# Optimization experiments

Measured on AMD Instinct MI355X. Metric: run time of the kernel, lower is better.

Reference implementation:

```python
import jax, jax.numpy as jnp
import numpy as np

N_NODES = 100000
N_EDGES = 600000
FEAT_DIM = 128


def setup_inputs() -> dict:
    key = jax.random.key(0)
    k_x, k_e, k_w1, k_b1, k_w2, k_b2 = jax.random.split(key, 6)
    x = jax.random.normal(k_x, (N_NODES, FEAT_DIM), dtype=jnp.float32)
    edge_index = jax.random.randint(k_e, (2, N_EDGES), 0, N_NODES, dtype=jnp.int64)
    # nn.Linear default init: U(-1/sqrt(fan_in), 1/sqrt(fan_in))
    lim1 = 1.0 / np.sqrt(2 * FEAT_DIM)
    lim2 = 1.0 / np.sqrt(FEAT_DIM)
    W1 = jax.random.uniform(k_w1, (2 * FEAT_DIM, FEAT_DIM), minval=-lim1, maxval=lim1, dtype=jnp.float32)
    b1 = jax.random.uniform(k_b1, (FEAT_DIM,), minval=-lim1, maxval=lim1, dtype=jnp.float32)
    W2 = jax.random.uniform(k_w2, (FEAT_DIM, 1), minval=-lim2, maxval=lim2, dtype=jnp.float32)
    b2 = jax.random.uniform(k_b2, (1,), minval=-lim2, maxval=lim2, dtype=jnp.float32)
    return {"x": x, "edge_index": edge_index, "W1": W1, "b1": b1, "W2": W2, "b2": b2}


def reference(x, edge_index, W1, b1, W2, b2):
    row, col = edge_index[0], edge_index[1]
    # gather endpoint features and concat -> [E, 2*feat_dim]
    edge_feat = jnp.concatenate([x[row], x[col]], axis=1)
    h = jax.nn.relu(edge_feat @ W1 + b1)  # [E, feat_dim]
    return jax.nn.sigmoid(h @ W2 + b2)    # [E, 1]
```

## Files before the change

kernel.cpp:

```cpp
#include <hip/hip_runtime.h>
#include <stdint.h>

#define N_NODES 100000
#define N_EDGES 600000
#define FEAT 128

typedef __attribute__((ext_vector_type(8))) short short8;
typedef __attribute__((ext_vector_type(4))) float floatx4;

__device__ __forceinline__ short f2bf(float f) {
    unsigned u = __builtin_bit_cast(unsigned, f);
    u = (u + 0x7FFFu + ((u >> 16) & 1u)) >> 16;
    return (short)u;
}
__device__ __forceinline__ float bf2f(short s) {
    unsigned u = ((unsigned)(unsigned short)s) << 16;
    return __builtin_bit_cast(float, u);
}

__global__ void cvt_w_kernel(const float* __restrict__ w1, short* __restrict__ wbt) {
    int i = blockIdx.x * 256 + threadIdx.x;
    int n = i >> 7, k = i & 127;
    float f = (n < FEAT) ? w1[k * FEAT + n] : w1[(FEAT + k) * FEAT + (n - FEAT)];
    wbt[i] = f2bf(f);
}

__global__ __launch_bounds__(256, 2) void node_gemm_kernel(
    const float* __restrict__ x, const short* __restrict__ wbt, short* __restrict__ y)
{
    __shared__ short lds_b[16 * 256 * 8];

    const int tid = threadIdx.x;
    for (int j = tid; j < 16 * 256; j += 256) {
        int n = j & 255, c = j >> 8;
        short8 v = *(const short8*)(wbt + n * 128 + c * 8);
        *(short8*)(lds_b + ((c << 8) + n) * 8) = v;
    }
    __syncthreads();

    const int lane = tid & 63;
    const int wave = tid >> 6;
    const int nl = lane & 15;
    const int q  = lane >> 4;
    const int m0 = blockIdx.x * 64 + wave * 16;

    const int node = m0 + nl;
    const int nsrc = (node < N_NODES) ? node : 0;
    short8 a[4];
#pragma unroll
    for (int s = 0; s < 4; ++s) {
        const float* p = x + (size_t)nsrc * FEAT + s * 32 + q * 8;
        short8 av;
#pragma unroll
        for (int j = 0; j < 8; ++j) av[j] = f2bf(p[j]);
        a[s] = av;
    }

    floatx4 acc[16];
#pragma unroll
    for (int nt = 0; nt < 16; ++nt) acc[nt] = (floatx4)(0.0f);

#pragma unroll
    for (int s = 0; s < 4; ++s) {
        const int crow = (s * 4 + q) << 8;
#pragma unroll
        for (int nt = 0; nt < 16; ++nt) {
            short8 bf = *(const short8*)(lds_b + ((crow + nt * 16 + nl) << 3));
            acc[nt] = __builtin_amdgcn_mfma_f32_16x16x32_bf16(a[s], bf, acc[nt], 0, 0, 0);
        }
    }

#pragma unroll
    for (int r = 0; r < 4; ++r) {
        int m = m0 + q * 4 + r;
        if (m >= N_NODES) continue;
        short* yr = y + (size_t)m * 256 + nl;
#pragma unroll
        for (int nt = 0; nt < 16; ++nt) yr[nt * 16] = f2bf(acc[nt][r]);
    }
}

__global__ __launch_bounds__(256) void edge_kernel(
    const short* __restrict__ y, const int* __restrict__ eidx,
    const float* __restrict__ b1, const float* __restrict__ w2,
    const float* __restrict__ b2, float* __restrict__ out)
{
    const int l = threadIdx.x & 15;

    float b1r[8], w2r[8];
#pragma unroll
    for (int j = 0; j < 8; ++j) {
        b1r[j] = b1[l * 8 + j];
        w2r[j] = w2[l * 8 + j];
    }
    const float bias2 = b2[0];

    const int slot   = blockIdx.x * 16 + (threadIdx.x >> 4);
    const int stride = gridDim.x * 16;

    for (int e = slot; e < N_EDGES; e += stride) {
        const int r = eidx[e];
        const int c = eidx[N_EDGES + e];

        short8 uu = *(const short8*)(y + (size_t)r * 256 + l * 8);
        short8 vv = *(const short8*)(y + (size_t)c * 256 + 128 + l * 8);

        float p = 0.0f;
#pragma unroll
        for (int j = 0; j < 8; ++j) {
            float h = bf2f(uu[j]) + bf2f(vv[j]) + b1r[j];
            p = fmaf(fmaxf(h, 0.0f), w2r[j], p);
        }
        p += __shfl_xor(p, 1);
        p += __shfl_xor(p, 2);
        p += __shfl_xor(p, 4);
        p += __shfl_xor(p, 8);

        if (l == 0) out[e] = 1.0f / (1.0f + __expf(-(p + bias2)));
    }
}

extern "C" void kernel_launch(void* const* d_in, const int* in_sizes, int n_in,
                              void* d_out, int out_size, void* d_ws, size_t ws_size,
                              hipStream_t stream) {
    const float* x  = (const float*)d_in[0];
    const int*   ei = (const int*)d_in[1];
    const float* W1 = (const float*)d_in[2];
    const float* b1 = (const float*)d_in[3];
    const float* W2 = (const float*)d_in[4];
    const float* b2 = (const float*)d_in[5];
    float* out = (float*)d_out;

    short* ybf = (short*)d_ws;
    short* wbt = ybf + (size_t)N_NODES * 256;

    cvt_w_kernel<<<32768 / 256, 256, 0, stream>>>(W1, wbt);

    int mblocks = (N_NODES + 63) / 64;
    node_gemm_kernel<<<mblocks, 256, 0, stream>>>(x, wbt, ybf);

    edge_kernel<<<2048, 256, 0, stream>>>(ybf, ei, b1, W2, b2, out);
}
```

Baseline: 166.1 us.

## Persistent split-N node GEMM with prefetch, swizzled LDS, and batched edge gathers

The node GEMM becomes a persistent grid where each block owns one 128-column half of W1. It keeps that half in an XOR-swizzled LDS layout, prefetches the next tile's x rows into registers during the MFMAs, and writes output with vectorized 4-wide stores with b1 folded in. The edge kernel drops the per-edge bias add and software-pipelines gathers four edges at a time, loading the next batch before computing the current one. This trades higher register pressure and a smaller per-block GEMM for better latency hiding and fewer LDS bank conflicts.

```diff
diff --git a/kernel.cpp b/kernel.cpp
--- a/kernel.cpp
+++ b/kernel.cpp
@@ -4,8 +4,12 @@
 #define N_NODES 100000
 #define N_EDGES 600000
 #define FEAT 128
+#define NTILES 1563
+#define NTASKS (NTILES * 2)
+#define GRID_G 1024
 
 typedef __attribute__((ext_vector_type(8))) short short8;
+typedef __attribute__((ext_vector_type(4))) short sv4;
 typedef __attribute__((ext_vector_type(4))) float floatx4;
 
 __device__ __forceinline__ short f2bf(float f) {
@@ -25,98 +29,158 @@
     wbt[i] = f2bf(f);
 }
 
-__global__ __launch_bounds__(256, 2) void node_gemm_kernel(
-    const float* __restrict__ x, const short* __restrict__ wbt, short* __restrict__ y)
+__global__ __launch_bounds__(256, 4) void node_gemm_kernel(
+    const float* __restrict__ x, const short* __restrict__ wbt,
+    const float* __restrict__ b1, short* __restrict__ y)
 {
-    __shared__ short lds_b[16 * 256 * 8];
-
-    const int tid = threadIdx.x;
-    for (int j = tid; j < 16 * 256; j += 256) {
-        int n = j & 255, c = j >> 8;
-        short8 v = *(const short8*)(wbt + n * 128 + c * 8);
-        *(short8*)(lds_b + ((c << 8) + n) * 8) = v;
-    }
-    __syncthreads();
-
+    __shared__ short lds_b[128 * 128];
+
+    const int tid  = threadIdx.x;
     const int lane = tid & 63;
     const int wave = tid >> 6;
-    const int nl = lane & 15;
-    const int q  = lane >> 4;
-    const int m0 = blockIdx.x * 64 + wave * 16;
-
-    const int node = m0 + nl;
-    const int nsrc = (node < N_NODES) ? node : 0;
-    short8 a[4];
-#pragma unroll
-    for (int s = 0; s < 4; ++s) {
-        const float* p = x + (size_t)nsrc * FEAT + s * 32 + q * 8;
-        short8 av;
-#pragma unroll
-        for (int j = 0; j < 8; ++j) av[j] = f2bf(p[j]);
-        a[s] = av;
-    }
-
-    floatx4 acc[16];
-#pragma unroll
-    for (int nt = 0; nt < 16; ++nt) acc[nt] = (floatx4)(0.0f);
-
-#pragma unroll
-    for (int s = 0; s < 4; ++s) {
-        const int crow = (s * 4 + q) << 8;
-#pragma unroll
-        for (int nt = 0; nt < 16; ++nt) {
-            short8 bf = *(const short8*)(lds_b + ((crow + nt * 16 + nl) << 3));
-            acc[nt] = __builtin_amdgcn_mfma_f32_16x16x32_bf16(a[s], bf, acc[nt], 0, 0, 0);
-        }
-    }
-
-#pragma unroll
-    for (int r = 0; r < 4; ++r) {
-        int m = m0 + q * 4 + r;
-        if (m >= N_NODES) continue;
-        short* yr = y + (size_t)m * 256 + nl;
-#pragma unroll
-        for (int nt = 0; nt < 16; ++nt) yr[nt * 16] = f2bf(acc[nt][r]);
+    const int nl   = lane & 15;
+    const int q    = lane >> 4;
+    const int swz  = nl & 7;
+    const int nh   = blockIdx.x & 1;
+
+#pragma unroll
+    for (int j0 = 0; j0 < 2048; j0 += 256) {
+        int j = j0 + tid;
+        int n = j >> 4, kc = j & 15;
+        short8 v = *(const short8*)(wbt + (nh * 128 + n) * 128 + kc * 8);
+        *(short8*)(lds_b + n * 128 + ((kc ^ (n & 7)) << 3)) = v;
+    }
+    __syncthreads();
+
+    int task = blockIdx.x;
+    float xf[32];
+    {
+        int node = (task >> 1) * 64 + wave * 16 + nl;
+        int nsrc = (node < N_NODES) ? node : 0;
+        const float* p = x + (size_t)nsrc * FEAT + q * 8;
+#pragma unroll
+        for (int s = 0; s < 4; ++s)
+#pragma unroll
+            for (int j = 0; j < 8; ++j) xf[s * 8 + j] = p[s * 32 + j];
+    }
+
+    for (; task < NTASKS; task += GRID_G) {
+        const int node = (task >> 1) * 64 + wave * 16 + nl;
+
+        short8 a[4];
+#pragma unroll
+        for (int s = 0; s < 4; ++s) {
+            short8 av;
+#pragma unroll
+            for (int j = 0; j < 8; ++j) av[j] = f2bf(xf[s * 8 + j]);
+            a[s] = av;
+        }
+
+        int task2 = task + GRID_G;
+        if (task2 < NTASKS) {
+            int node2 = (task2 >> 1) * 64 + wave * 16 + nl;
+            int nsrc = (node2 < N_NODES) ? node2 : 0;
+            const float* p = x + (size_t)nsrc * FEAT + q * 8;
+#pragma unroll
+            for (int s = 0; s < 4; ++s)
+#pragma unroll
+                for (int j = 0; j < 8; ++j) xf[s * 8 + j] = p[s * 32 + j];
+        }
+
+        floatx4 acc[8];
+#pragma unroll
+        for (int nt = 0; nt < 8; ++nt) acc[nt] = (floatx4)(0.0f);
+
+#pragma unroll
+        for (int s = 0; s < 4; ++s) {
+            const int koff = ((s * 4 + q) ^ swz) << 3;
+#pragma unroll
+            for (int nt = 0; nt < 8; ++nt) {
+                short8 af = *(const short8*)(lds_b + (nt * 16 + nl) * 128 + koff);
+                acc[nt] = __builtin_amdgcn_mfma_f32_16x16x32_bf16(af, a[s], acc[nt], 0, 0, 0);
+            }
+        }
+
+        if (node < N_NODES) {
+            short* yr = y + (size_t)node * 256 + nh * 128 + q * 4;
+            if (nh == 0) {
+#pragma unroll
+                for (int nt = 0; nt < 8; ++nt) {
+                    floatx4 bb = *(const floatx4*)(b1 + nt * 16 + q * 4);
+                    sv4 o;
+                    o[0] = f2bf(acc[nt][0] + bb[0]); o[1] = f2bf(acc[nt][1] + bb[1]);
+                    o[2] = f2bf(acc[nt][2] + bb[2]); o[3] = f2bf(acc[nt][3] + bb[3]);
+                    *(sv4*)(yr + nt * 16) = o;
+                }
+            } else {
+#pragma unroll
+                for (int nt = 0; nt < 8; ++nt) {
+                    sv4 o;
+                    o[0] = f2bf(acc[nt][0]); o[1] = f2bf(acc[nt][1]);
+                    o[2] = f2bf(acc[nt][2]); o[3] = f2bf(acc[nt][3]);
+                    *(sv4*)(yr + nt * 16) = o;
+                }
+            }
+        }
     }
 }
 
 __global__ __launch_bounds__(256) void edge_kernel(
     const short* __restrict__ y, const int* __restrict__ eidx,
-    const float* __restrict__ b1, const float* __restrict__ w2,
-    const float* __restrict__ b2, float* __restrict__ out)
+    const float* __restrict__ w2, const float* __restrict__ b2,
+    float* __restrict__ out)
 {
     const int l = threadIdx.x & 15;
 
-    float b1r[8], w2r[8];
-#pragma unroll
-    for (int j = 0; j < 8; ++j) {
-        b1r[j] = b1[l * 8 + j];
-        w2r[j] = w2[l * 8 + j];
-    }
+    float w2r[8];
+#pragma unroll
+    for (int j = 0; j < 8; ++j) w2r[j] = w2[l * 8 + j];
     const float bias2 = b2[0];
 
     const int slot   = blockIdx.x * 16 + (threadIdx.x >> 4);
     const int stride = gridDim.x * 16;
 
-    for (int e = slot; e < N_EDGES; e += stride) {
-        const int r = eidx[e];
-        const int c = eidx[N_EDGES + e];
-
-        short8 uu = *(const short8*)(y + (size_t)r * 256 + l * 8);
-        short8 vv = *(const short8*)(y + (size_t)c * 256 + 128 + l * 8);
-
-        float p = 0.0f;
-#pragma unroll
-        for (int j = 0; j < 8; ++j) {
-            float h = bf2f(uu[j]) + bf2f(vv[j]) + b1r[j];
-            p = fmaf(fmaxf(h, 0.0f), w2r[j], p);
-        }
-        p += __shfl_xor(p, 1);
-        p += __shfl_xor(p, 2);
-        p += __shfl_xor(p, 4);
-        p += __shfl_xor(p, 8);
-
-        if (l == 0) out[e] = 1.0f / (1.0f + __expf(-(p + bias2)));
+    short8 cu[4], cv[4], nu[4], nv[4];
+#pragma unroll
+    for (int b = 0; b < 4; ++b) {
+        int e = slot + b * stride;
+        if (e < N_EDGES) {
+            int r = eidx[e], c = eidx[N_EDGES + e];
+            cu[b] = *(const short8*)(y + (size_t)r * 256 + l * 8);
+            cv[b] = *(const short8*)(y + (size_t)c * 256 + 128 + l * 8);
+        }
+    }
+
+    for (int eb = slot; eb < N_EDGES; eb += 4 * stride) {
+        int nb = eb + 4 * stride;
+#pragma unroll
+        for (int b = 0; b < 4; ++b) {
+            int e = nb + b * stride;
+            if (e < N_EDGES) {
+                int r = eidx[e], c = eidx[N_EDGES + e];
+                nu[b] = *(const short8*)(y + (size_t)r * 256 + l * 8);
+                nv[b] = *(const short8*)(y + (size_t)c * 256 + 128 + l * 8);
+            }
+        }
+#pragma unroll
+        for (int b = 0; b < 4; ++b) {
+            int e = eb + b * stride;
+            if (e < N_EDGES) {
+                float p = 0.0f;
+#pragma unroll
+                for (int j = 0; j < 8; ++j) {
+                    float h = bf2f(cu[b][j]) + bf2f(cv[b][j]);
+                    p = fmaf(fmaxf(h, 0.0f), w2r[j], p);
+                }
+                p += __shfl_xor(p, 1);
+                p += __shfl_xor(p, 2);
+                p += __shfl_xor(p, 4);
+                p += __shfl_xor(p, 8);
+                if (l == 0) out[e] = 1.0f / (1.0f + __expf(-(p + bias2)));
+            }
+        }
+#pragma unroll
+        for (int b = 0; b < 4; ++b) { cu[b] = nu[b]; cv[b] = nv[b]; }
     }
 }
 
@@ -135,9 +199,6 @@
     short* wbt = ybf + (size_t)N_NODES * 256;
 
     cvt_w_kernel<<<32768 / 256, 256, 0, stream>>>(W1, wbt);
-
-    int mblocks = (N_NODES + 63) / 64;
-    node_gemm_kernel<<<mblocks, 256, 0, stream>>>(x, wbt, ybf);
-
-    edge_kernel<<<2048, 256, 0, stream>>>(ybf, ei, b1, W2, b2, out);
-}
+    node_gemm_kernel<<<GRID_G, 256, 0, stream>>>(x, wbt, b1, ybf);
+    edge_kernel<<<2048, 256, 0, stream>>>(ybf, ei, W2, b2, out);
+}
```

Measured after the change: 242.0 us. +45.7%, slower.

## Prefetch edge gathers in batches, fold b1 into node GEMM, enlarge GEMM blocks

Applied to the files above, without the earlier changes.

The edge kernel now processes four edges per thread group per iteration and issues the gathers for the next batch before computing the current one. This raises memory-level parallelism to hide the latency of random gathers. The first layer's bias b1 is added in the node GEMM epilogue before the bf16 store, which removes a per-edge add and the b1 register loads. The node GEMM grows to 512-thread blocks of 128 rows so the weight staging into LDS is shared across more rows. The risks are higher register pressure from the double-buffered short8 arrays and a small rounding change, since the bias is now rounded into bf16.

```diff
diff --git a/kernel.cpp b/kernel.cpp
--- a/kernel.cpp
+++ b/kernel.cpp
@@ -4,6 +4,7 @@
 #define N_NODES 100000
 #define N_EDGES 600000
 #define FEAT 128
+#define BLK_M 128
 
 typedef __attribute__((ext_vector_type(8))) short short8;
 typedef __attribute__((ext_vector_type(4))) float floatx4;
@@ -25,13 +26,14 @@
     wbt[i] = f2bf(f);
 }
 
-__global__ __launch_bounds__(256, 2) void node_gemm_kernel(
-    const float* __restrict__ x, const short* __restrict__ wbt, short* __restrict__ y)
+__global__ __launch_bounds__(512, 4) void node_gemm_kernel(
+    const float* __restrict__ x, const short* __restrict__ wbt,
+    const float* __restrict__ b1, short* __restrict__ y)
 {
     __shared__ short lds_b[16 * 256 * 8];
 
     const int tid = threadIdx.x;
-    for (int j = tid; j < 16 * 256; j += 256) {
+    for (int j = tid; j < 16 * 256; j += 512) {
         int n = j & 255, c = j >> 8;
         short8 v = *(const short8*)(wbt + n * 128 + c * 8);
         *(short8*)(lds_b + ((c << 8) + n) * 8) = v;
@@ -42,7 +44,7 @@
     const int wave = tid >> 6;
     const int nl = lane & 15;
     const int q  = lane >> 4;
-    const int m0 = blockIdx.x * 64 + wave * 16;
+    const int m0 = blockIdx.x * BLK_M + wave * 16;
 
     const int node = m0 + nl;
     const int nsrc = (node < N_NODES) ? node : 0;
@@ -55,6 +57,10 @@
         for (int j = 0; j < 8; ++j) av[j] = f2bf(p[j]);
         a[s] = av;
     }
+
+    float b1v[8];
+#pragma unroll
+    for (int nt = 0; nt < 8; ++nt) b1v[nt] = b1[nt * 16 + nl];
 
     floatx4 acc[16];
 #pragma unroll
@@ -76,47 +82,68 @@
         if (m >= N_NODES) continue;
         short* yr = y + (size_t)m * 256 + nl;
 #pragma unroll
-        for (int nt = 0; nt < 16; ++nt) yr[nt * 16] = f2bf(acc[nt][r]);
+        for (int nt = 0; nt < 8; ++nt) yr[nt * 16] = f2bf(acc[nt][r] + b1v[nt]);
+#pragma unroll
+        for (int nt = 8; nt < 16; ++nt) yr[nt * 16] = f2bf(acc[nt][r]);
     }
 }
 
 __global__ __launch_bounds__(256) void edge_kernel(
     const short* __restrict__ y, const int* __restrict__ eidx,
-    const float* __restrict__ b1, const float* __restrict__ w2,
-    const float* __restrict__ b2, float* __restrict__ out)
+    const float* __restrict__ w2, const float* __restrict__ b2,
+    float* __restrict__ out)
 {
     const int l = threadIdx.x & 15;
 
-    float b1r[8], w2r[8];
+    float w2r[8];
 #pragma unroll
-    for (int j = 0; j < 8; ++j) {
-        b1r[j] = b1[l * 8 + j];
-        w2r[j] = w2[l * 8 + j];
-    }
+    for (int j = 0; j < 8; ++j) w2r[j] = w2[l * 8 + j];
     const float bias2 = b2[0];
 
     const int slot   = blockIdx.x * 16 + (threadIdx.x >> 4);
     const int stride = gridDim.x * 16;
 
-    for (int e = slot; e < N_EDGES; e += stride) {
-        const int r = eidx[e];
-        const int c = eidx[N_EDGES + e];
+    short8 cu[4], cv[4], nu[4], nv[4];
+#pragma unroll
+    for (int b = 0; b < 4; ++b) {
+        int e = slot + b * stride;
+        if (e < N_EDGES) {
+            int r = eidx[e], c = eidx[N_EDGES + e];
+            cu[b] = *(const short8*)(y + (size_t)r * 256 + l * 8);
+            cv[b] = *(const short8*)(y + (size_t)c * 256 + 128 + l * 8);
+        }
+    }
 
-        short8 uu = *(const short8*)(y + (size_t)r * 256 + l * 8);
-        short8 vv = *(const short8*)(y + (size_t)c * 256 + 128 + l * 8);
-
-        float p = 0.0f;
+    for (int eb = slot; eb < N_EDGES; eb += 4 * stride) {
+        int nb = eb + 4 * stride;
 #pragma unroll
-        for (int j = 0; j < 8; ++j) {
-            float h = bf2f(uu[j]) + bf2f(vv[j]) + b1r[j];
-            p = fmaf(fmaxf(h, 0.0f), w2r[j], p);
+        for (int b = 0; b < 4; ++b) {
+            int e = nb + b * stride;
+            if (e < N_EDGES) {
+                int r = eidx[e], c = eidx[N_EDGES + e];
+                nu[b] = *(const short8*)(y + (size_t)r * 256 + l * 8);
+                nv[b] = *(const short8*)(y + (size_t)c * 256 + 128 + l * 8);
+            }
         }
-        p += __shfl_xor(p, 1);
-        p += __shfl_xor(p, 2);
-        p += __shfl_xor(p, 4);
-        p += __shfl_xor(p, 8);
-
-        if (l == 0) out[e] = 1.0f / (1.0f + __expf(-(p + bias2)));
+#pragma unroll
+        for (int b = 0; b < 4; ++b) {
+            int e = eb + b * stride;
+            if (e < N_EDGES) {
+                float p = 0.0f;
+#pragma unroll
+                for (int j = 0; j < 8; ++j) {
+                    float h = bf2f(cu[b][j]) + bf2f(cv[b][j]);
+                    p = fmaf(fmaxf(h, 0.0f), w2r[j], p);
+                }
+                p += __shfl_xor(p, 1);
+                p += __shfl_xor(p, 2);
+                p += __shfl_xor(p, 4);
+                p += __shfl_xor(p, 8);
+                if (l == 0) out[e] = 1.0f / (1.0f + __expf(-(p + bias2)));
+            }
+        }
+#pragma unroll
+        for (int b = 0; b < 4; ++b) { cu[b] = nu[b]; cv[b] = nv[b]; }
     }
 }
 
@@ -136,8 +163,8 @@
 
     cvt_w_kernel<<<32768 / 256, 256, 0, stream>>>(W1, wbt);
 
-    int mblocks = (N_NODES + 63) / 64;
-    node_gemm_kernel<<<mblocks, 256, 0, stream>>>(x, wbt, ybf);
+    int mblocks = (N_NODES + BLK_M - 1) / BLK_M;
+    node_gemm_kernel<<<mblocks, 512, 0, stream>>>(x, wbt, b1, ybf);
 
-    edge_kernel<<<2048, 256, 0, stream>>>(ybf, ei, b1, W2, b2, out);
+    edge_kernel<<<2048, 256, 0, stream>>>(ybf, ei, W2, b2, out);
 }
```

After: 167.2 us. Within noise of the previous version (+0.7%).
